# Kernel optimization log

Hardware: AMD Instinct MI355X
Metric: run time of the kernel (lower is better)

## Reference

```python
import jax, jax.numpy as jnp
import numpy as np

B, C, H, W = 8, 64, 128, 128


def _conv3x3(x, w, b):
    # x: [B,C,H,W], w: [O,I,3,3], b: [O]; stride 1, padding 1
    y = jax.lax.conv_general_dilated(
        x, w, window_strides=(1, 1), padding=((1, 1), (1, 1)),
        dimension_numbers=('NCHW', 'OIHW', 'NCHW'))
    return y + b[None, :, None, None]


def setup_inputs() -> dict:
    key = jax.random.key(0)
    ks = jax.random.split(key, 8)
    s = 0.05
    return {
        'x': jax.random.normal(ks[0], (B, C, H, W), jnp.float32),
        'Wq': jax.random.normal(ks[1], (C, C, 3, 3), jnp.float32) * s,
        'bq': jax.random.normal(ks[2], (C,), jnp.float32) * s,
        'Wk': jax.random.normal(ks[3], (C, C, 3, 3), jnp.float32) * s,
        'bk': jax.random.normal(ks[4], (C,), jnp.float32) * s,
        'Wv': jax.random.normal(ks[5], (C, C, 3, 3), jnp.float32) * s,
        'bv': jax.random.normal(ks[6], (C,), jnp.float32) * s,
        'gamma': jax.random.normal(ks[7], (1,), jnp.float32) * s,
    }


def reference(x, Wq, bq, Wk, bk, Wv, bv, gamma):
    b_, c_, h_, w_ = x.shape
    q = _conv3x3(x, Wq, bq)  # [B,C,H,W]
    k = _conv3x3(x, Wk, bk)
    v = _conv3x3(x, Wv, bv)

    # energy along H (column attention): eH[b,h,w,g] = sum_c q[b,c,h,w]*k[b,c,g,w]
    eH = jnp.einsum('bchw,bcgw->bhwg', q, k)
    eye = jnp.eye(h_, dtype=bool)  # mask diagonal h==g with -inf
    eH = jnp.where(eye[None, :, None, :], -jnp.inf, eH)

    # energy along W (row attention): eW[b,h,w,g] = sum_c q[b,c,h,w]*k[b,c,h,g]
    eW = jnp.einsum('bchw,bchg->bhwg', q, k)

    # joint softmax over concatenated [H | W] axis
    att = jax.nn.softmax(jnp.concatenate([eH, eW], axis=3), axis=3)
    att_H = att[:, :, :, :h_]          # [B,H,W,H]
    att_W = att[:, :, :, h_:h_ + w_]   # [B,H,W,W]

    out_H = jnp.einsum('bcgw,bhwg->bchw', v, att_H)
    out_W = jnp.einsum('bchg,bhwg->bchw', v, att_W)

    return gamma[0] * (out_H + out_W) + x
```

## Files before the change

### kernel.cpp

```cpp
#include <hip/hip_runtime.h>
#include <hip/hip_bf16.h>

#define B_ 8
#define C_ 64
#define H_ 128
#define W_ 128
#define HW_  ((size_t)H_ * W_)
#define CHW_ ((size_t)C_ * H_ * W_)

typedef unsigned short u16;
typedef unsigned int   u32;
typedef __attribute__((ext_vector_type(8))) short bf16x8;
typedef __attribute__((ext_vector_type(4))) float f32x4;

__device__ __forceinline__ float bf2f(u16 h) {
    union { u32 u; float f; } c; c.u = ((u32)h) << 16; return c.f;
}
__device__ __forceinline__ u16 f2bf(float f) {
    union { float f; u32 u; } c; c.f = f;
    u32 u = c.u;
    u32 r = (u + 0x7fffu + ((u >> 16) & 1u)) >> 16;
    return (u16)r;
}
__device__ __forceinline__ u32 pack2(float a, float b) {
    return (u32)f2bf(a) | ((u32)f2bf(b) << 16);
}
__device__ __forceinline__ float sanit(float x, float lo, float hi) {
    return fminf(fmaxf(x, lo), hi);
}
__device__ __forceinline__ void gload_lds16(const u16* g, u16* l) {
    __builtin_amdgcn_global_load_lds(
        (const __attribute__((address_space(1))) void*)g,
        (__attribute__((address_space(3))) void*)l, 16, 0, 0);
}

__global__ __launch_bounds__(256) void prep_weights(
    const float* __restrict__ Wq, const float* __restrict__ Wk,
    const float* __restrict__ Wv, u16* __restrict__ Wt)
{
    int tap = blockIdx.x;
    int cog = blockIdx.y * 4 + (threadIdx.x >> 6);
    int ci  = threadIdx.x & 63;
    int arr = cog >> 6, co = cog & 63;
    const float* src = arr == 0 ? Wq : (arr == 1 ? Wk : Wv);
    Wt[tap * 12288 + cog * 64 + ci] = f2bf(src[(co * 64 + ci) * 9 + tap]);
}

__global__ __launch_bounds__(256) void xprep_kernel(
    const float* __restrict__ x, u16* __restrict__ xb)
{
    const int hp  = blockIdx.x;
    const int tid = threadIdx.x;
    u16* dst = xb + ((size_t)blockIdx.y * 130 + hp) * 8192;
    if (hp == 0 || hp == 129) {
#pragma unroll
        for (int i = 0; i < 4; i++)
            *(uint4*)(dst + (size_t)(tid + i * 256) * 8) = (uint4){0, 0, 0, 0};
        return;
    }
    const float* xr = x + (size_t)blockIdx.y * CHW_ + (size_t)(hp - 1) * W_;
#pragma unroll
    for (int it = 0; it < 4; it++) {
        int idx = tid + it * 256;
        int px  = idx & 127;
        int g   = idx >> 7;
        float vb[8];
#pragma unroll
        for (int e = 0; e < 8; e++)
            vb[e] = xr[(size_t)(g * 8 + e) * HW_ + px];
        uint4 o;
        o.x = pack2(vb[0], vb[1]);
        o.y = pack2(vb[2], vb[3]);
        o.z = pack2(vb[4], vb[5]);
        o.w = pack2(vb[6], vb[7]);
        *(uint4*)(dst + (size_t)(g * 128 + px) * 8) = o;
    }
}

__global__ __launch_bounds__(256, 2) void conv_mfma_kernel(
    const u16* __restrict__ xb, const u16* __restrict__ Wt,
    const float* __restrict__ bq, const float* __restrict__ bk,
    const float* __restrict__ bv,
    u16* __restrict__ qN, u16* __restrict__ kN, u16* __restrict__ v)
{
    const int nwg  = gridDim.x * gridDim.y;
    const int flat = blockIdx.y * gridDim.x + blockIdx.x;
    const int wg   = (flat & 7) * (nwg >> 3) + (flat >> 3);
    const int h    = wg & (H_ - 1);
    const int bidx = wg >> 7;
    const size_t boff = (size_t)bidx * CHW_;
    const int tid  = threadIdx.x;
    const int lane = tid & 63, wv = tid >> 6;
    const int ln15 = lane & 15, quad = lane >> 4;

    __shared__ __align__(16) u16 xI[24960];

    const int woff = (wv * 16 + ln15) * 64 + quad * 8;

    bf16x8 wcur[2][3], wnxt[2][3];
#pragma unroll
    for (int ks = 0; ks < 2; ks++)
#pragma unroll
        for (int mt = 0; mt < 3; mt++)
            wcur[ks][mt] = *(const bf16x8*)(Wt + woff + mt * 4096 + ks * 32);

    if (tid < 48) {
        int dh = tid >> 4, g = (tid & 15) >> 1, p = (tid & 1) ? 129 : 0;
        *(uint4*)(xI + dh * 8320 + g * 1040 + p * 8) = (uint4){0, 0, 0, 0};
    }

    const u16* xrows = xb + ((size_t)bidx * 130 + h) * 8192;
#pragma unroll
    for (int it = 0; it < 12; it++) {
        int chunk = wv * 12 + it;
        int dh = chunk >> 4, g = (chunk >> 1) & 7, half = chunk & 1;
        gload_lds16(xrows + (size_t)dh * 8192 + g * 1024 + half * 512 + lane * 8,
                    xI + dh * 8320 + g * 1040 + 8 + half * 512);
    }
    __syncthreads();

    f32x4 acc[3][8];
#pragma unroll
    for (int mt = 0; mt < 3; mt++)
#pragma unroll
        for (int nt = 0; nt < 8; nt++)
            acc[mt][nt] = (f32x4){0.f, 0.f, 0.f, 0.f};

#pragma unroll
    for (int tap = 0; tap < 9; tap++) {
        const int dh = tap / 3, dw = tap % 3;
        if (tap < 8) {
#pragma unroll
            for (int ks = 0; ks < 2; ks++)
#pragma unroll
                for (int mt = 0; mt < 3; mt++)
                    wnxt[ks][mt] = *(const bf16x8*)(Wt + (tap + 1) * 12288 + woff + mt * 4096 + ks * 32);
        }
        const u16* xrow = xI + dh * 8320;
#pragma unroll
        for (int ks = 0; ks < 2; ks++) {
            bf16x8 bfr[8];
#pragma unroll
            for (int nt = 0; nt < 8; nt++)
                bfr[nt] = *(const bf16x8*)(xrow + ((quad + ks * 4) * 1040 + (nt * 16 + ln15 + dw) * 8));
            __builtin_amdgcn_s_setprio(1);
#pragma unroll
            for (int mt = 0; mt < 3; mt++)
#pragma unroll
                for (int nt = 0; nt < 8; nt++)
                    acc[mt][nt] = __builtin_amdgcn_mfma_f32_16x16x32_bf16(
                        wcur[ks][mt], bfr[nt], acc[mt][nt], 0, 0, 0);
            __builtin_amdgcn_s_setprio(0);
        }
        if (tap < 8) {
#pragma unroll
            for (int ks = 0; ks < 2; ks++)
#pragma unroll
                for (int mt = 0; mt < 3; mt++)
                    wcur[ks][mt] = wnxt[ks][mt];
        }
    }

    const int cb = wv * 16 + quad * 4;
#pragma unroll
    for (int mt = 0; mt < 3; mt++) {
        const float* bias = mt == 0 ? bq : (mt == 1 ? bk : bv);
        float b0 = bias[cb], b1 = bias[cb + 1], b2 = bias[cb + 2], b3 = bias[cb + 3];
        if (mt < 2) {
            u16* dst = (mt ? kN : qN) + boff + (size_t)h * W_ * 64 + cb;
#pragma unroll
            for (int nt = 0; nt < 8; nt++) {
                int px = nt * 16 + ln15;
                u32 p0 = pack2(acc[mt][nt][0] + b0, acc[mt][nt][1] + b1);
                u32 p1 = pack2(acc[mt][nt][2] + b2, acc[mt][nt][3] + b3);
                *(u32*)(dst + (size_t)px * 64)     = p0;
                *(u32*)(dst + (size_t)px * 64 + 2) = p1;
            }
        } else {
            float bb[4] = {b0, b1, b2, b3};
#pragma unroll
            for (int r = 0; r < 4; r++) {
                u16* drow = v + boff + (size_t)(cb + r) * HW_ + (size_t)h * W_;
#pragma unroll
                for (int nt = 0; nt < 8; nt++)
                    drow[nt * 16 + ln15] = f2bf(acc[mt][nt][r] + bb[r]);
            }
        }
    }
}

__global__ __launch_bounds__(256) void vt_kernel(
    const u16* __restrict__ v, u16* __restrict__ vT)
{
    __shared__ u16 Ts[64 * 72];
    const u16* src = v  + (size_t)blockIdx.z * CHW_ + (size_t)blockIdx.y * HW_;
    u16* dst       = vT + (size_t)blockIdx.z * CHW_ + (size_t)blockIdx.y * HW_;
    const int ti = blockIdx.x & 1, tj = blockIdx.x >> 1;
    const int r0 = ti * 64, c0 = tj * 64;
    const int tid = threadIdx.x;
    const int r = tid >> 2, cq = tid & 3;
#pragma unroll
    for (int i = 0; i < 2; i++) {
        uint4 u = *(const uint4*)(src + (size_t)(r0 + r) * 128 + c0 + cq * 16 + i * 8);
        *(uint4*)(Ts + r * 72 + cq * 16 + i * 8) = u;
    }
    __syncthreads();
    const int wr = tid >> 2, hq = tid & 3;
    union { u16 o[16]; uint4 v4[2]; } t;
#pragma unroll
    for (int j = 0; j < 16; j++) t.o[j] = Ts[(hq * 16 + j) * 72 + wr];
    *(uint4*)(dst + (size_t)(c0 + wr) * 128 + r0 + hq * 16)     = t.v4[0];
    *(uint4*)(dst + (size_t)(c0 + wr) * 128 + r0 + hq * 16 + 8) = t.v4[1];
}

__global__ __launch_bounds__(256, 4) void col_kernel(
    const u16* __restrict__ qN, const u16* __restrict__ kN,
    const u16* __restrict__ vT,
    float* __restrict__ maxH, float* __restrict__ sumH,
    u16* __restrict__ Ocol)
{
    const size_t boff = (size_t)blockIdx.z * CHW_;
    const size_t soff = (size_t)blockIdx.z * HW_;
    qN += boff; kN += boff; vT += boff; Ocol += boff;
    maxH += soff; sumH += soff;

    const int s    = blockIdx.x;
    const int tid  = threadIdx.x;
    const int lane = tid & 63, wv = tid >> 6;
    const int ln15 = lane & 15, quad = lane >> 4;

    __shared__ __align__(16) u16 smemU[18432];
    u16* Qs = smemU;
    u16* Ks = smemU + 9216;

#pragma unroll
    for (int it = 0; it < 4; it++) {
        int idx = tid + it * 256;
        int t = idx >> 3, cg = (idx & 7) * 8;
        size_t off = (size_t)t * 8192 + (size_t)s * 64 + cg;
        *(uint4*)(Qs + t * 72 + cg) = *(const uint4*)(qN + off);
        *(uint4*)(Ks + t * 72 + cg) = *(const uint4*)(kN + off);
    }
    __syncthreads();

    f32x4 Sc[2][8];
#pragma unroll
    for (int tt = 0; tt < 2; tt++)
#pragma unroll
        for (int gt = 0; gt < 8; gt++)
            Sc[tt][gt] = (f32x4){0.f, 0.f, 0.f, 0.f};

#pragma unroll
    for (int ks = 0; ks < 2; ks++) {
        bf16x8 bq_[2];
#pragma unroll
        for (int tt = 0; tt < 2; tt++)
            bq_[tt] = *(const bf16x8*)(Qs + ((wv * 2 + tt) * 16 + ln15) * 72 + ks * 32 + quad * 8);
#pragma unroll
        for (int gt = 0; gt < 8; gt++) {
            bf16x8 ak = *(const bf16x8*)(Ks + (gt * 16 + ln15) * 72 + ks * 32 + quad * 8);
#pragma unroll
            for (int tt = 0; tt < 2; tt++)
                Sc[tt][gt] = __builtin_amdgcn_mfma_f32_16x16x32_bf16(ak, bq_[tt], Sc[tt][gt], 0, 0, 0);
        }
    }

    const int tb[2] = { (wv * 2) * 16 + ln15, (wv * 2 + 1) * 16 + ln15 };
#pragma unroll
    for (int tt = 0; tt < 2; tt++)
#pragma unroll
        for (int gt = 0; gt < 8; gt++)
#pragma unroll
            for (int r = 0; r < 4; r++)
                if (gt * 16 + quad * 4 + r == tb[tt]) Sc[tt][gt][r] = -1e30f;

#pragma unroll
    for (int tt = 0; tt < 2; tt++) {
        float m = Sc[tt][0][0];
#pragma unroll
        for (int gt = 0; gt < 8; gt++)
#pragma unroll
            for (int r = 0; r < 4; r++) m = fmaxf(m, Sc[tt][gt][r]);
        m = fmaxf(m, __shfl_xor(m, 16));
        m = fmaxf(m, __shfl_xor(m, 32));
        float ss = 0.f;
#pragma unroll
        for (int gt = 0; gt < 8; gt++)
#pragma unroll
            for (int r = 0; r < 4; r++) {
                float e = __expf(Sc[tt][gt][r] - m);
                ss += e;
                Sc[tt][gt][r] = e;
            }
        ss += __shfl_xor(ss, 16);
        ss += __shfl_xor(ss, 32);
        if (quad == 0) {
            int pix = tb[tt] * W_ + s;
            maxH[pix] = m; sumH[pix] = ss;
        }
    }
    __syncthreads();
    u16* Ps = smemU;
#pragma unroll
    for (int tt = 0; tt < 2; tt++)
#pragma unroll
        for (int gt = 0; gt < 8; gt++)
#pragma unroll
            for (int r = 0; r < 4; r++)
                Ps[tb[tt] * 136 + gt * 16 + quad * 4 + r] = f2bf(Sc[tt][gt][r]);
    __syncthreads();

    f32x4 Oc[2][4];
#pragma unroll
    for (int mt = 0; mt < 2; mt++)
#pragma unroll
        for (int nt = 0; nt < 4; nt++)
            Oc[mt][nt] = (f32x4){0.f, 0.f, 0.f, 0.f};
#pragma unroll
    for (int kg = 0; kg < 4; kg++) {
        bf16x8 ap[2];
#pragma unroll
        for (int mt = 0; mt < 2; mt++)
            ap[mt] = *(const bf16x8*)(Ps + (wv * 32 + mt * 16 + ln15) * 136 + kg * 32 + quad * 8);
#pragma unroll
        for (int nt = 0; nt < 4; nt++) {
            bf16x8 bv_ = *(const bf16x8*)(vT + (size_t)(nt * 16 + ln15) * HW_ + (size_t)s * 128 + kg * 32 + quad * 8);
#pragma unroll
            for (int mt = 0; mt < 2; mt++)
                Oc[mt][nt] = __builtin_amdgcn_mfma_f32_16x16x32_bf16(ap[mt], bv_, Oc[mt][nt], 0, 0, 0);
        }
    }
    __syncthreads();
    u16* OfU = smemU;
#pragma unroll
    for (int mt = 0; mt < 2; mt++)
#pragma unroll
        for (int nt = 0; nt < 4; nt++)
#pragma unroll
            for (int r = 0; r < 4; r++)
                OfU[(wv * 32 + mt * 16 + quad * 4 + r) * 72 + nt * 16 + ln15] = f2bf(Oc[mt][nt][r]);
    __syncthreads();
#pragma unroll
    for (int it = 0; it < 4; it++) {
        int idx = tid + it * 256;
        int t = idx >> 3, c8 = (idx & 7) * 8;
        *(uint4*)(Ocol + ((size_t)t * 128 + s) * 64 + c8) = *(uint4*)(OfU + t * 72 + c8);
    }
}

__global__ __launch_bounds__(256, 4) void row_kernel(
    const u16* __restrict__ qN, const u16* __restrict__ kN,
    const u16* __restrict__ v,
    const float* __restrict__ x, const float* __restrict__ gammap,
    const float* __restrict__ maxH, const float* __restrict__ sumH,
    const u16* __restrict__ Ocol, float* __restrict__ out)
{
    const size_t boff = (size_t)blockIdx.z * CHW_;
    const size_t soff = (size_t)blockIdx.z * HW_;
    qN += boff; kN += boff; v += boff; Ocol += boff; x += boff; out += boff;
    maxH += soff; sumH += soff;

    const int s    = blockIdx.x;
    const int tid  = threadIdx.x;
    const int lane = tid & 63, wv = tid >> 6;
    const int ln15 = lane & 15, quad = lane >> 4;

    __shared__ __align__(16) u16 smemU[18432];
    u16* Qs = smemU;
    u16* Ks = smemU + 9216;
    float* alL = (float*)(smemU + 17408);

    const int tb[2] = { (wv * 2) * 16 + ln15, (wv * 2 + 1) * 16 + ln15 };
    float mcv[2], scv[2];
#pragma unroll
    for (int tt = 0; tt < 2; tt++) {
        mcv[tt] = maxH[s * W_ + tb[tt]];
        scv[tt] = sumH[s * W_ + tb[tt]];
    }

#pragma unroll
    for (int it = 0; it < 4; it++) {
        int idx = tid + it * 256;
        int t = idx >> 3, cg = (idx & 7) * 8;
        size_t off = (size_t)s * 8192 + (size_t)t * 64 + cg;
        *(uint4*)(Qs + t * 72 + cg) = *(const uint4*)(qN + off);
        *(uint4*)(Ks + t * 72 + cg) = *(const uint4*)(kN + off);
    }
    __syncthreads();

    f32x4 Sc[2][8];
#pragma unroll
    for (int tt = 0; tt < 2; tt++)
#pragma unroll
        for (int gt = 0; gt < 8; gt++)
            Sc[tt][gt] = (f32x4){0.f, 0.f, 0.f, 0.f};
#pragma unroll
    for (int ks = 0; ks < 2; ks++) {
        bf16x8 bq_[2];
#pragma unroll
        for (int tt = 0; tt < 2; tt++)
            bq_[tt] = *(const bf16x8*)(Qs + ((wv * 2 + tt) * 16 + ln15) * 72 + ks * 32 + quad * 8);
#pragma unroll
        for (int gt = 0; gt < 8; gt++) {
            bf16x8 ak = *(const bf16x8*)(Ks + (gt * 16 + ln15) * 72 + ks * 32 + quad * 8);
#pragma unroll
            for (int tt = 0; tt < 2; tt++)
                Sc[tt][gt] = __builtin_amdgcn_mfma_f32_16x16x32_bf16(ak, bq_[tt], Sc[tt][gt], 0, 0, 0);
        }
    }

    float be[2];
#pragma unroll
    for (int tt = 0; tt < 2; tt++) {
        float m = Sc[tt][0][0];
#pragma unroll
        for (int gt = 0; gt < 8; gt++)
#pragma unroll
            for (int r = 0; r < 4; r++) m = fmaxf(m, Sc[tt][gt][r]);
        m = fmaxf(m, __shfl_xor(m, 16));
        m = fmaxf(m, __shfl_xor(m, 32));
        float ss = 0.f;
#pragma unroll
        for (int gt = 0; gt < 8; gt++)
#pragma unroll
            for (int r = 0; r < 4; r++) {
                float e = __expf(Sc[tt][gt][r] - m);
                ss += e;
                Sc[tt][gt][r] = e;
            }
        ss += __shfl_xor(ss, 16);
        ss += __shfl_xor(ss, 32);
        float mc = sanit(mcv[tt], -3e38f, 3e38f);
        float sc = sanit(scv[tt], 0.f, 3e38f);
        float mm = fmaxf(mc, m);
        float dd = sc * __expf(fminf(mc - mm, 0.f)) + ss * __expf(m - mm);
        float rv = 1.0f / fmaxf(dd, 1e-30f);
        be[tt] = __expf(m - mm) * rv;
        if (quad == 0) alL[tb[tt]] = __expf(fminf(mc - mm, 0.f)) * rv;
    }
    __syncthreads();
    u16* Ps = smemU;
#pragma unroll
    for (int tt = 0; tt < 2; tt++)
#pragma unroll
        for (int gt = 0; gt < 8; gt++)
#pragma unroll
            for (int r = 0; r < 4; r++)
                Ps[tb[tt] * 136 + gt * 16 + quad * 4 + r] = f2bf(Sc[tt][gt][r] * be[tt]);
    __syncthreads();

    f32x4 Oc[2][4];
#pragma unroll
    for (int mt = 0; mt < 2; mt++)
#pragma unroll
        for (int nt = 0; nt < 4; nt++)
            Oc[mt][nt] = (f32x4){0.f, 0.f, 0.f, 0.f};
#pragma unroll
    for (int kg = 0; kg < 4; kg++) {
        bf16x8 ap[2];
#pragma unroll
        for (int mt = 0; mt < 2; mt++)
            ap[mt] = *(const bf16x8*)(Ps + (wv * 32 + mt * 16 + ln15) * 136 + kg * 32 + quad * 8);
#pragma unroll
        for (int nt = 0; nt < 4; nt++) {
            bf16x8 bv_ = *(const bf16x8*)(v + (size_t)(nt * 16 + ln15) * HW_ + (size_t)s * 128 + kg * 32 + quad * 8);
#pragma unroll
            for (int mt = 0; mt < 2; mt++)
                Oc[mt][nt] = __builtin_amdgcn_mfma_f32_16x16x32_bf16(ap[mt], bv_, Oc[mt][nt], 0, 0, 0);
        }
    }
    __syncthreads();

    const float gmm = gammap[0];
    float* Of = (float*)smemU;
#pragma unroll
    for (int mt = 0; mt < 2; mt++)
#pragma unroll
        for (int nt = 0; nt < 4; nt++) {
            float fv[4];
            int c = nt * 16 + ln15;
#pragma unroll
            for (int r = 0; r < 4; r++) {
                int tt = wv * 32 + mt * 16 + quad * 4 + r;
                float oc = bf2f(Ocol[((size_t)s * 128 + tt) * 64 + c]);
                fv[r] = gmm * (Oc[mt][nt][r] + alL[tt] * oc);
            }
            int w0 = wv * 32 + mt * 16 + quad * 4;
            *(float4*)(Of + c * 132 + w0) = make_float4(fv[0], fv[1], fv[2], fv[3]);
        }
    __syncthreads();
    int c = tid >> 2, w0 = (tid & 3) * 32;
#pragma unroll
    for (int i = 0; i < 8; i++) {
        int w = w0 + i * 4;
        float4 xo = *(const float4*)(x + (size_t)c * HW_ + (size_t)s * 128 + w);
        float4 of = *(const float4*)(Of + c * 132 + w);
        *(float4*)(out + (size_t)c * HW_ + (size_t)s * 128 + w) =
            make_float4(of.x + xo.x, of.y + xo.y, of.z + xo.z, of.w + xo.w);
    }
}

extern "C" void kernel_launch(void* const* d_in, const int* in_sizes, int n_in,
                              void* d_out, int out_size, void* d_ws, size_t ws_size,
                              hipStream_t stream)
{
    const float* x  = (const float*)d_in[0];
    const float* Wq = (const float*)d_in[1];
    const float* bq = (const float*)d_in[2];
    const float* Wk = (const float*)d_in[3];
    const float* bk = (const float*)d_in[4];
    const float* Wv = (const float*)d_in[5];
    const float* bv = (const float*)d_in[6];
    const float* gm = (const float*)d_in[7];
    float* out = (float*)d_out;

    char* ws = (char*)d_ws;
    const size_t need1 = 4 * (size_t)B_ * CHW_ * 2 + (size_t)B_ * CHW_ * 4
                       + 2 * (size_t)B_ * HW_ * 4 + 221184;
    int passes = (ws_size >= need1) ? 1 : 2;
    int nb = B_ / passes;

    const size_t SL = (size_t)nb * CHW_ * 2;
    const size_t OC = (size_t)nb * CHW_ * 4;
    const size_t ST = (size_t)nb * HW_ * 4;
    u16*   qNb  = (u16*)(ws);
    u16*   kNb  = (u16*)(ws + SL);
    u16*   v    = (u16*)(ws + 2 * SL);
    u16*   vT   = (u16*)(ws + 3 * SL);
    u16*   Ocol = (u16*)(ws + 4 * SL);
    float* maxH = (float*)(ws + 4 * SL + OC);
    float* sumH = (float*)(ws + 4 * SL + OC + ST);
    u16*   Wt   = (u16*)(ws + 4 * SL + OC + 2 * ST);
    u16*   xb   = (u16*)Ocol;

    dim3 blk(256);
    prep_weights<<<dim3(9, 48), blk, 0, stream>>>(Wq, Wk, Wv, Wt);

    for (int p = 0; p < passes; p++) {
        const float* xbp = x + (size_t)p * nb * CHW_;
        float* ob = out + (size_t)p * nb * CHW_;
        xprep_kernel<<<dim3(130, nb), blk, 0, stream>>>(xbp, xb);
        conv_mfma_kernel<<<dim3(H_, nb), blk, 0, stream>>>(xb, Wt, bq, bk, bv, qNb, kNb, v);
        vt_kernel<<<dim3(4, C_, nb), blk, 0, stream>>>(v, vT);
        col_kernel<<<dim3(W_, 1, nb), blk, 0, stream>>>(qNb, kNb, vT, maxH, sumH, Ocol);
        row_kernel<<<dim3(H_, 1, nb), blk, 0, stream>>>(qNb, kNb, v, xbp, gm, maxH, sumH, Ocol, ob);
    }
}
```

Baseline: 188.7 us.

## Retile conv kernel to 4 rows by half-width per block; pack softmax LDS stores

The conv kernel now has each workgroup cover four output rows and one 64-pixel half of the width. It stages six input rows (with halo) in LDS once and computes two passes of two rows each, so each input row is reused across vertically adjacent outputs and fewer redundant row loads are made. The grid shrinks from 128 to 64 blocks per batch. The col and row kernels also pack four bf16 probabilities into a single 8-byte LDS store instead of four scalar stores. The trade-off is fewer workgroups, slightly more LDS per block, and weights reloaded per pass.

```diff
diff --git a/kernel.cpp b/kernel.cpp
--- a/kernel.cpp
+++ b/kernel.cpp
@@ -86,104 +86,123 @@
     const int nwg  = gridDim.x * gridDim.y;
     const int flat = blockIdx.y * gridDim.x + blockIdx.x;
     const int wg   = (flat & 7) * (nwg >> 3) + (flat >> 3);
-    const int h    = wg & (H_ - 1);
-    const int bidx = wg >> 7;
+    const int p    = wg & 1;
+    const int hq   = (wg >> 1) & 31;
+    const int bidx = wg >> 6;
+    const int h0   = hq * 4;
     const size_t boff = (size_t)bidx * CHW_;
     const int tid  = threadIdx.x;
     const int lane = tid & 63, wv = tid >> 6;
     const int ln15 = lane & 15, quad = lane >> 4;
 
-    __shared__ __align__(16) u16 xI[24960];
+    __shared__ __align__(16) u16 xI[26112];
 
     const int woff = (wv * 16 + ln15) * 64 + quad * 8;
 
-    bf16x8 wcur[2][3], wnxt[2][3];
-#pragma unroll
-    for (int ks = 0; ks < 2; ks++)
-#pragma unroll
-        for (int mt = 0; mt < 3; mt++)
-            wcur[ks][mt] = *(const bf16x8*)(Wt + woff + mt * 4096 + ks * 32);
-
+    const u16* xrow0 = xb + ((size_t)bidx * 130 + h0) * 8192;
+#pragma unroll
+    for (int it = 0; it < 12; it++) {
+        int unit = wv * 12 + it;
+        int i = unit >> 3, g = unit & 7;
+        const u16* src = xrow0 + (size_t)i * 8192 + g * 1024 + p * 512 - 16;
+        u16* dst = xI + (i * 8 + g) * 544;
+        gload_lds16(src + lane * 8, dst);
+        gload_lds16(src + 32 + lane * 8, dst + 32);
+    }
+    __syncthreads();
     if (tid < 48) {
-        int dh = tid >> 4, g = (tid & 15) >> 1, p = (tid & 1) ? 129 : 0;
-        *(uint4*)(xI + dh * 8320 + g * 1040 + p * 8) = (uint4){0, 0, 0, 0};
-    }
-
-    const u16* xrows = xb + ((size_t)bidx * 130 + h) * 8192;
-#pragma unroll
-    for (int it = 0; it < 12; it++) {
-        int chunk = wv * 12 + it;
-        int dh = chunk >> 4, g = (chunk >> 1) & 7, half = chunk & 1;
-        gload_lds16(xrows + (size_t)dh * 8192 + g * 1024 + half * 512 + lane * 8,
-                    xI + dh * 8320 + g * 1040 + 8 + half * 512);
-    }
-    __syncthreads();
-
-    f32x4 acc[3][8];
-#pragma unroll
-    for (int mt = 0; mt < 3; mt++)
-#pragma unroll
-        for (int nt = 0; nt < 8; nt++)
-            acc[mt][nt] = (f32x4){0.f, 0.f, 0.f, 0.f};
-
-#pragma unroll
-    for (int tap = 0; tap < 9; tap++) {
-        const int dh = tap / 3, dw = tap % 3;
-        if (tap < 8) {
-#pragma unroll
-            for (int ks = 0; ks < 2; ks++)
-#pragma unroll
-                for (int mt = 0; mt < 3; mt++)
-                    wnxt[ks][mt] = *(const bf16x8*)(Wt + (tap + 1) * 12288 + woff + mt * 4096 + ks * 32);
-        }
-        const u16* xrow = xI + dh * 8320;
-#pragma unroll
-        for (int ks = 0; ks < 2; ks++) {
-            bf16x8 bfr[8];
-#pragma unroll
-            for (int nt = 0; nt < 8; nt++)
-                bfr[nt] = *(const bf16x8*)(xrow + ((quad + ks * 4) * 1040 + (nt * 16 + ln15 + dw) * 8));
-            __builtin_amdgcn_s_setprio(1);
+        int i = tid >> 3, g = tid & 7;
+        int slot = p ? 66 : 1;
+        *(uint4*)(xI + (i * 8 + g) * 544 + slot * 8) = (uint4){0, 0, 0, 0};
+    }
+    __syncthreads();
+
+    const int cb = wv * 16 + quad * 4;
+    float bqv[4], bkv[4], bvv[4];
+#pragma unroll
+    for (int r = 0; r < 4; r++) {
+        bqv[r] = bq[cb + r]; bkv[r] = bk[cb + r]; bvv[r] = bv[cb + r];
+    }
+
+#pragma unroll
+    for (int pass = 0; pass < 2; pass++) {
+        f32x4 acc[2][3][4];
+#pragma unroll
+        for (int hh = 0; hh < 2; hh++)
 #pragma unroll
             for (int mt = 0; mt < 3; mt++)
 #pragma unroll
-                for (int nt = 0; nt < 8; nt++)
-                    acc[mt][nt] = __builtin_amdgcn_mfma_f32_16x16x32_bf16(
-                        wcur[ks][mt], bfr[nt], acc[mt][nt], 0, 0, 0);
-            __builtin_amdgcn_s_setprio(0);
-        }
-        if (tap < 8) {
-#pragma unroll
-            for (int ks = 0; ks < 2; ks++)
-#pragma unroll
-                for (int mt = 0; mt < 3; mt++)
-                    wcur[ks][mt] = wnxt[ks][mt];
-        }
-    }
-
-    const int cb = wv * 16 + quad * 4;
-#pragma unroll
-    for (int mt = 0; mt < 3; mt++) {
-        const float* bias = mt == 0 ? bq : (mt == 1 ? bk : bv);
-        float b0 = bias[cb], b1 = bias[cb + 1], b2 = bias[cb + 2], b3 = bias[cb + 3];
-        if (mt < 2) {
-            u16* dst = (mt ? kN : qN) + boff + (size_t)h * W_ * 64 + cb;
-#pragma unroll
-            for (int nt = 0; nt < 8; nt++) {
-                int px = nt * 16 + ln15;
-                u32 p0 = pack2(acc[mt][nt][0] + b0, acc[mt][nt][1] + b1);
-                u32 p1 = pack2(acc[mt][nt][2] + b2, acc[mt][nt][3] + b3);
-                *(u32*)(dst + (size_t)px * 64)     = p0;
-                *(u32*)(dst + (size_t)px * 64 + 2) = p1;
-            }
-        } else {
-            float bb[4] = {b0, b1, b2, b3};
+                for (int nt = 0; nt < 4; nt++)
+                    acc[hh][mt][nt] = (f32x4){0.f, 0.f, 0.f, 0.f};
+
+        bf16x8 wcur[2][3], wnxt[2][3];
+#pragma unroll
+        for (int ks = 0; ks < 2; ks++)
+#pragma unroll
+            for (int mt = 0; mt < 3; mt++)
+                wcur[ks][mt] = *(const bf16x8*)(Wt + woff + mt * 4096 + ks * 32);
+
+#pragma unroll
+        for (int tap = 0; tap < 9; tap++) {
+            const int dh = tap / 3, dw = tap % 3;
+            if (tap < 8) {
+#pragma unroll
+                for (int ks = 0; ks < 2; ks++)
+#pragma unroll
+                    for (int mt = 0; mt < 3; mt++)
+                        wnxt[ks][mt] = *(const bf16x8*)(Wt + (tap + 1) * 12288 + woff + mt * 4096 + ks * 32);
+            }
+#pragma unroll
+            for (int hh = 0; hh < 2; hh++) {
+                const int row = pass * 2 + hh + dh;
+#pragma unroll
+                for (int ks = 0; ks < 2; ks++) {
+                    bf16x8 bfr[4];
+#pragma unroll
+                    for (int nt = 0; nt < 4; nt++)
+                        bfr[nt] = *(const bf16x8*)(xI + (row * 8 + quad + ks * 4) * 544
+                                                      + (nt * 16 + ln15 + 1 + dw) * 8);
+                    __builtin_amdgcn_s_setprio(1);
+#pragma unroll
+                    for (int mt = 0; mt < 3; mt++)
+#pragma unroll
+                        for (int nt = 0; nt < 4; nt++)
+                            acc[hh][mt][nt] = __builtin_amdgcn_mfma_f32_16x16x32_bf16(
+                                wcur[ks][mt], bfr[nt], acc[hh][mt][nt], 0, 0, 0);
+                    __builtin_amdgcn_s_setprio(0);
+                }
+            }
+            if (tap < 8) {
+#pragma unroll
+                for (int ks = 0; ks < 2; ks++)
+#pragma unroll
+                    for (int mt = 0; mt < 3; mt++)
+                        wcur[ks][mt] = wnxt[ks][mt];
+            }
+        }
+
+#pragma unroll
+        for (int hh = 0; hh < 2; hh++) {
+            const int h = h0 + pass * 2 + hh;
+#pragma unroll
+            for (int mt = 0; mt < 2; mt++) {
+                const float* bb = mt == 0 ? bqv : bkv;
+                u16* dst = (mt ? kN : qN) + boff + (size_t)h * W_ * 64 + cb;
+#pragma unroll
+                for (int nt = 0; nt < 4; nt++) {
+                    int px = p * 64 + nt * 16 + ln15;
+                    u32 p0 = pack2(acc[hh][mt][nt][0] + bb[0], acc[hh][mt][nt][1] + bb[1]);
+                    u32 p1 = pack2(acc[hh][mt][nt][2] + bb[2], acc[hh][mt][nt][3] + bb[3]);
+                    *(u32*)(dst + (size_t)px * 64)     = p0;
+                    *(u32*)(dst + (size_t)px * 64 + 2) = p1;
+                }
+            }
 #pragma unroll
             for (int r = 0; r < 4; r++) {
                 u16* drow = v + boff + (size_t)(cb + r) * HW_ + (size_t)h * W_;
 #pragma unroll
-                for (int nt = 0; nt < 8; nt++)
-                    drow[nt * 16 + ln15] = f2bf(acc[mt][nt][r] + bb[r]);
+                for (int nt = 0; nt < 4; nt++)
+                    drow[p * 64 + nt * 16 + ln15] = f2bf(acc[hh][2][nt][r] + bvv[r]);
             }
         }
     }
@@ -304,10 +323,11 @@
 #pragma unroll
     for (int tt = 0; tt < 2; tt++)
 #pragma unroll
-        for (int gt = 0; gt < 8; gt++)
-#pragma unroll
-            for (int r = 0; r < 4; r++)
-                Ps[tb[tt] * 136 + gt * 16 + quad * 4 + r] = f2bf(Sc[tt][gt][r]);
+        for (int gt = 0; gt < 8; gt++) {
+            u32 lo = pack2(Sc[tt][gt][0], Sc[tt][gt][1]);
+            u32 hi = pack2(Sc[tt][gt][2], Sc[tt][gt][3]);
+            *(uint2*)(Ps + tb[tt] * 136 + gt * 16 + quad * 4) = make_uint2(lo, hi);
+        }
     __syncthreads();
 
     f32x4 Oc[2][4];
@@ -443,10 +463,11 @@
 #pragma unroll
     for (int tt = 0; tt < 2; tt++)
 #pragma unroll
-        for (int gt = 0; gt < 8; gt++)
-#pragma unroll
-            for (int r = 0; r < 4; r++)
-                Ps[tb[tt] * 136 + gt * 16 + quad * 4 + r] = f2bf(Sc[tt][gt][r] * be[tt]);
+        for (int gt = 0; gt < 8; gt++) {
+            u32 lo = pack2(Sc[tt][gt][0] * be[tt], Sc[tt][gt][1] * be[tt]);
+            u32 hi = pack2(Sc[tt][gt][2] * be[tt], Sc[tt][gt][3] * be[tt]);
+            *(uint2*)(Ps + tb[tt] * 136 + gt * 16 + quad * 4) = make_uint2(lo, hi);
+        }
     __syncthreads();
 
     f32x4 Oc[2][4];
@@ -540,7 +561,7 @@
         const float* xbp = x + (size_t)p * nb * CHW_;
         float* ob = out + (size_t)p * nb * CHW_;
         xprep_kernel<<<dim3(130, nb), blk, 0, stream>>>(xbp, xb);
-        conv_mfma_kernel<<<dim3(H_, nb), blk, 0, stream>>>(xb, Wt, bq, bk, bv, qNb, kNb, v);
+        conv_mfma_kernel<<<dim3(64, nb), blk, 0, stream>>>(xb, Wt, bq, bk, bv, qNb, kNb, v);
         vt_kernel<<<dim3(4, C_, nb), blk, 0, stream>>>(v, vT);
         col_kernel<<<dim3(W_, 1, nb), blk, 0, stream>>>(qNb, kNb, vT, maxH, sumH, Ocol);
         row_kernel<<<dim3(H_, 1, nb), blk, 0, stream>>>(qNb, kNb, v, xbp, gm, maxH, sumH, Ocol, ob);
```

New measurement: 187.2 us. No clear change (-0.8%).
